# Performance work log

Hardware: AMD Instinct MI355X
Metric: run time of the kernel (lower is better)

The kernel has to match this reference:

```python
import jax, jax.numpy as jnp
import numpy as np

T, H, F, E, K = 1024, 2048, 1024, 8, 2  # tokens, hidden, intermediate, experts, top_k
RENORMALIZE = True


def setup_inputs() -> dict:
    key = jax.random.key(0)
    k1, k2, k3, k4, k5 = jax.random.split(key, 5)
    hidden_states = jax.random.normal(k1, (T, H), dtype=jnp.float32)
    router_logits = jax.random.normal(k2, (T, E), dtype=jnp.float32)
    w1 = jax.random.normal(k3, (E, H, F), dtype=jnp.float32) * 0.02  # gate proj
    w3 = jax.random.normal(k4, (E, H, F), dtype=jnp.float32) * 0.02  # up proj
    w2 = jax.random.normal(k5, (E, F, H), dtype=jnp.float32) * 0.02  # down proj
    return {"hidden_states": hidden_states, "router_logits": router_logits,
            "w1": w1, "w3": w3, "w2": w2}


def _moe_forward(x, router_logits, w1, w3, w2):
    # Top-K routing: softmax over all experts, select top-k, optional renormalize.
    probs = jax.nn.softmax(router_logits, axis=-1)            # [T, E]
    topk_vals, topk_ids = jax.lax.top_k(probs, K)             # [T, K]
    if RENORMALIZE:
        topk_vals = topk_vals / jnp.sum(topk_vals, axis=-1, keepdims=True)
    # Dense combine weights: zero for non-selected experts.   [T, E]
    tok_idx = jnp.arange(x.shape[0])[:, None]
    combine = jnp.zeros(probs.shape, dtype=x.dtype).at[tok_idx, topk_ids].set(topk_vals)
    # Expert SwiGLU FFN computed per expert over all tokens, masked-combined.
    g = jnp.einsum('th,ehf->etf', x, w1)                      # gate  [E, T, F]
    u = jnp.einsum('th,ehf->etf', x, w3)                      # up    [E, T, F]
    a = jax.nn.silu(g) * u                                    # silu activation
    y = jnp.einsum('etf,efh->eth', a, w2)                     # down  [E, T, H]
    out = jnp.einsum('eth,te->th', y, combine)                # weighted combine
    return out


def reference(hidden_states, router_logits, w1, w3, w2):
    return _moe_forward(hidden_states, router_logits, w1, w3, w2)
```

## Files before the change

### kernel.cpp

```cpp
#include <hip/hip_runtime.h>
#include <cstdint>
#include <cstddef>

#define T_TOK 1024
#define H_DIM 2048
#define F_DIM 1024
#define E_EXP 8
#define BM 64
#define BK 64
#define BN1 32
#define BN2 64
#define SP 70
#define MAX_TILES 40
#define ROWCAP 2560

#define I_NTILES 25
#define I_TILE_E 32
#define I_TILE_R0 80
#define I_ROWTOK 4224
#define I_ROWW   6784
#define B_XB     37888
#define B_AWS    (37888 + T_TOK*H_DIM*2)

typedef __bf16 bf16x8 __attribute__((ext_vector_type(8)));
typedef __bf16 bf16x4 __attribute__((ext_vector_type(4)));
typedef __bf16 bf16x2 __attribute__((ext_vector_type(2)));
typedef float  f32x4  __attribute__((ext_vector_type(4)));

#define MFMA(a,b,c) __builtin_amdgcn_mfma_f32_16x16x32_bf16(a,b,c,0,0,0)

__global__ __launch_bounds__(1024) void k_route(const float* __restrict__ logits,
                                                int* __restrict__ ws_i) {
  __shared__ int cnt[E_EXP], cur[E_EXP], offs_s[E_EXP];
  const int t = threadIdx.x;
  float* ws_f = (float*)ws_i;
  if (t < E_EXP) { cnt[t] = 0; cur[t] = 0; }
  __syncthreads();
  float l[E_EXP];
#pragma unroll
  for (int e = 0; e < E_EXP; ++e) l[e] = logits[t * E_EXP + e];
  int b0 = 0; float v0 = l[0];
#pragma unroll
  for (int e = 1; e < E_EXP; ++e) if (l[e] > v0) { v0 = l[e]; b0 = e; }
  int b1 = -1; float v1 = -3.4e38f;
#pragma unroll
  for (int e = 0; e < E_EXP; ++e) if (e != b0 && l[e] > v1) { v1 = l[e]; b1 = e; }
  float w0 = 1.f / (1.f + __expf(v1 - v0));
  float w1 = 1.f - w0;
  atomicAdd(&cnt[b0], 1);
  atomicAdd(&cnt[b1], 1);
  __syncthreads();
  if (t == 0) {
    int off = 0, nt = 0;
    for (int e = 0; e < E_EXP; ++e) {
      offs_s[e] = off;
      int ntile = (cnt[e] + BM - 1) / BM;
      for (int i = 0; i < ntile; ++i) {
        ws_i[I_TILE_E + nt] = e;
        ws_i[I_TILE_R0 + nt] = off + i * BM;
        ++nt;
      }
      off += ntile * BM;
    }
    ws_i[I_NTILES] = nt;
  }
  for (int i = t; i < ROWCAP; i += 1024) ws_i[I_ROWTOK + i] = -1;
  __syncthreads();
  {
    int p = atomicAdd(&cur[b0], 1);
    int s = offs_s[b0] + p;
    ws_i[I_ROWTOK + s] = t;
    ws_f[I_ROWW + s] = w0;
  }
  {
    int p = atomicAdd(&cur[b1], 1);
    int s = offs_s[b1] + p;
    ws_i[I_ROWTOK + s] = t;
    ws_f[I_ROWW + s] = w1;
  }
}

__global__ __launch_bounds__(256) void k_cvt(const float* __restrict__ x,
                                             __bf16* __restrict__ xb) {
  long i = (long)(blockIdx.x * 256 + threadIdx.x) * 8;
  float4 a = *(const float4*)(x + i);
  float4 b = *(const float4*)(x + i + 4);
  bf16x8 v;
  v[0] = (__bf16)a.x; v[1] = (__bf16)a.y; v[2] = (__bf16)a.z; v[3] = (__bf16)a.w;
  v[4] = (__bf16)b.x; v[5] = (__bf16)b.y; v[6] = (__bf16)b.z; v[7] = (__bf16)b.w;
  *(bf16x8*)(xb + i) = v;
}

__global__ __launch_bounds__(256) void k_gemm1(const __bf16* __restrict__ xb,
                                               const float* __restrict__ w1,
                                               const float* __restrict__ w3,
                                               const int* __restrict__ ws_i,
                                               __bf16* __restrict__ aws) {
  __shared__ __bf16 As[BM][SP];
  __shared__ __bf16 B1s[BN1][SP];
  __shared__ __bf16 B3s[BN1][SP];
  __shared__ int s_tok[BM];
  const int p = blockIdx.x;
  const int lg = (p & 7) * 160 + (p >> 3);
  const int tile = lg % MAX_TILES;
  const int n0 = (lg / MAX_TILES) * BN1;
  if (tile >= ws_i[I_NTILES]) return;
  const int e  = ws_i[I_TILE_E + tile];
  const int r0 = ws_i[I_TILE_R0 + tile];
  const int tid = threadIdx.x, lane = tid & 63, wid = tid >> 6;
  const int wm = wid;
  const int l15 = lane & 15, lk8 = (lane >> 4) << 3;
  const int ar = tid >> 3, ac = (tid & 7) * 8;
  const int nb = (tid & 7) * 4, kq = (tid >> 3) * 2;
  if (tid < BM) {
    int tk = ws_i[I_ROWTOK + r0 + tid];
    s_tok[tid] = tk < 0 ? 0 : tk;
  }
  __syncthreads();
  const int tok0 = s_tok[ar], tok1 = s_tok[ar + 32];
  const __bf16* xA0 = xb + (size_t)tok0 * H_DIM + ac;
  const __bf16* xA1 = xb + (size_t)tok1 * H_DIM + ac;
  const float* pB1 = w1 + (size_t)e * H_DIM * F_DIM + n0 + nb + (size_t)kq * F_DIM;
  const float* pB3 = w3 + (size_t)e * H_DIM * F_DIM + n0 + nb + (size_t)kq * F_DIM;

  bf16x8 rA0, rA1;
  f32x4 q1[2], q3[2];
  f32x4 accg[2] = {}; f32x4 accu[2] = {};

  auto LOADG = [&](int K0) {
    rA0 = *(const bf16x8*)(xA0 + K0);
    rA1 = *(const bf16x8*)(xA1 + K0);
#pragma unroll
    for (int j = 0; j < 2; ++j) {
      q1[j] = *(const f32x4*)(pB1 + (size_t)(K0 + j) * F_DIM);
      q3[j] = *(const f32x4*)(pB3 + (size_t)(K0 + j) * F_DIM);
    }
  };
  auto WRITEL = [&]() {
    *(bf16x8*)&As[ar][ac] = rA0;
    *(bf16x8*)&As[ar + 32][ac] = rA1;
#pragma unroll
    for (int u = 0; u < 4; ++u) {
      bf16x2 v1, v3;
      v1[0] = (__bf16)q1[0][u]; v1[1] = (__bf16)q1[1][u];
      v3[0] = (__bf16)q3[0][u]; v3[1] = (__bf16)q3[1][u];
      *(bf16x2*)&B1s[nb + u][kq] = v1;
      *(bf16x2*)&B3s[nb + u][kq] = v3;
    }
  };

  LOADG(0);
  for (int k0 = 0; k0 < H_DIM; k0 += BK) {
    if (k0) __syncthreads();
    WRITEL();
    if (k0 + BK < H_DIM) LOADG(k0 + BK);
    __syncthreads();
    __builtin_amdgcn_s_setprio(1);
#pragma unroll
    for (int kk = 0; kk < 2; ++kk) {
      const int kb = kk * 32 + lk8;
      bf16x8 a   = *(const bf16x8*)&As[wm * 16 + l15][kb];
      bf16x8 b10 = *(const bf16x8*)&B1s[l15][kb];
      bf16x8 b11 = *(const bf16x8*)&B1s[16 + l15][kb];
      bf16x8 b30 = *(const bf16x8*)&B3s[l15][kb];
      bf16x8 b31 = *(const bf16x8*)&B3s[16 + l15][kb];
      accg[0] = MFMA(a, b10, accg[0]);
      accg[1] = MFMA(a, b11, accg[1]);
      accu[0] = MFMA(a, b30, accu[0]);
      accu[1] = MFMA(a, b31, accu[1]);
    }
    __builtin_amdgcn_s_setprio(0);
  }
#pragma unroll
  for (int fn = 0; fn < 2; ++fn)
#pragma unroll
    for (int r = 0; r < 4; ++r) {
      float g = accg[fn][r], u = accu[fn][r];
      float a = g / (1.f + __expf(-g)) * u;
      int row = r0 + wm * 16 + ((lane >> 4) << 2) + r;
      int col = n0 + fn * 16 + l15;
      aws[(size_t)row * F_DIM + col] = (__bf16)a;
    }
}

__global__ __launch_bounds__(256) void k_gemm2(const __bf16* __restrict__ aws,
                                               const float* __restrict__ w2,
                                               const int* __restrict__ ws_i,
                                               float* __restrict__ out) {
  __shared__ __bf16 As[BM][SP];
  __shared__ __bf16 Bs[BN2][SP];
  __shared__ int s_tok[BM];
  __shared__ float s_w[BM];
  const int p = blockIdx.x;
  const int lg = (p & 7) * 160 + (p >> 3);
  const int tile = lg % MAX_TILES;
  const int h0 = (lg / MAX_TILES) * BN2;
  if (tile >= ws_i[I_NTILES]) return;
  const int e  = ws_i[I_TILE_E + tile];
  const int r0 = ws_i[I_TILE_R0 + tile];
  const int tid = threadIdx.x, lane = tid & 63, wid = tid >> 6;
  const int wm = wid >> 1, wn = wid & 1;
  const int l15 = lane & 15, lk8 = (lane >> 4) << 3;
  const int ar = tid >> 3, ac = (tid & 7) * 8;
  const int nb = (tid & 15) * 4, kq = (tid >> 4) * 4;
  const float* ws_f = (const float*)ws_i;
  if (tid < BM) {
    s_tok[tid] = ws_i[I_ROWTOK + r0 + tid];
    s_w[tid]   = ws_f[I_ROWW + r0 + tid];
  }
  __syncthreads();
  const __bf16* pA0 = aws + (size_t)(r0 + ar) * F_DIM + ac;
  const __bf16* pA1 = aws + (size_t)(r0 + ar + 32) * F_DIM + ac;
  const float* pB2 = w2 + (size_t)e * F_DIM * H_DIM + h0 + nb + (size_t)kq * H_DIM;

  bf16x8 rA0, rA1;
  f32x4 q2[4];
  auto LOADG = [&](int K0) {
    rA0 = *(const bf16x8*)(pA0 + K0);
    rA1 = *(const bf16x8*)(pA1 + K0);
#pragma unroll
    for (int j = 0; j < 4; ++j) q2[j] = *(const f32x4*)(pB2 + (size_t)(K0 + j) * H_DIM);
  };
  auto WRITEL = [&]() {
    *(bf16x8*)&As[ar][ac] = rA0;
    *(bf16x8*)&As[ar + 32][ac] = rA1;
#pragma unroll
    for (int u = 0; u < 4; ++u) {
      bf16x2 va, vb;
      va[0] = (__bf16)q2[0][u]; va[1] = (__bf16)q2[1][u];
      vb[0] = (__bf16)q2[2][u]; vb[1] = (__bf16)q2[3][u];
      *(bf16x2*)&Bs[nb + u][kq] = va;
      *(bf16x2*)&Bs[nb + u][kq + 2] = vb;
    }
  };

  f32x4 acc[2][2] = {};
  LOADG(0);
  for (int k0 = 0; k0 < F_DIM; k0 += BK) {
    if (k0) __syncthreads();
    WRITEL();
    if (k0 + BK < F_DIM) LOADG(k0 + BK);
    __syncthreads();
    __builtin_amdgcn_s_setprio(1);
#pragma unroll
    for (int kk = 0; kk < 2; ++kk) {
      const int kb = kk * 32 + lk8;
      bf16x8 a0 = *(const bf16x8*)&As[wm * 32 + l15][kb];
      bf16x8 a1 = *(const bf16x8*)&As[wm * 32 + 16 + l15][kb];
      bf16x8 b0 = *(const bf16x8*)&Bs[wn * 32 + l15][kb];
      bf16x8 b1 = *(const bf16x8*)&Bs[wn * 32 + 16 + l15][kb];
      acc[0][0] = MFMA(a0, b0, acc[0][0]);
      acc[0][1] = MFMA(a0, b1, acc[0][1]);
      acc[1][0] = MFMA(a1, b0, acc[1][0]);
      acc[1][1] = MFMA(a1, b1, acc[1][1]);
    }
    __builtin_amdgcn_s_setprio(0);
  }
#pragma unroll
  for (int fm = 0; fm < 2; ++fm)
#pragma unroll
    for (int fn = 0; fn < 2; ++fn)
#pragma unroll
      for (int r = 0; r < 4; ++r) {
        int lrow = wm * 32 + fm * 16 + ((lane >> 4) << 2) + r;
        int t = s_tok[lrow];
        if (t >= 0) {
          float v = acc[fm][fn][r] * s_w[lrow];
          atomicAdd(out + (size_t)t * H_DIM + h0 + wn * 32 + fn * 16 + l15, v);
        }
      }
}

extern "C" void kernel_launch(void* const* d_in, const int* in_sizes, int n_in,
                              void* d_out, int out_size, void* d_ws, size_t ws_size,
                              hipStream_t stream) {
  (void)in_sizes; (void)n_in; (void)out_size; (void)ws_size;
  const float* x      = (const float*)d_in[0];
  const float* logits = (const float*)d_in[1];
  const float* w1     = (const float*)d_in[2];
  const float* w3     = (const float*)d_in[3];
  const float* w2     = (const float*)d_in[4];
  float* out = (float*)d_out;
  int* ws_i = (int*)d_ws;
  __bf16* xb  = (__bf16*)((char*)d_ws + B_XB);
  __bf16* aws = (__bf16*)((char*)d_ws + B_AWS);

  hipMemsetAsync(d_out, 0, (size_t)T_TOK * H_DIM * sizeof(float), stream);
  k_route<<<1, 1024, 0, stream>>>(logits, ws_i);
  k_cvt<<<dim3(T_TOK * H_DIM / (256 * 8)), 256, 0, stream>>>(x, xb);
  k_gemm1<<<dim3(MAX_TILES * (F_DIM / BN1)), 256, 0, stream>>>(xb, w1, w3, ws_i, aws);
  k_gemm2<<<dim3(MAX_TILES * (H_DIM / BN2)), 256, 0, stream>>>(aws, w2, ws_i, out);
}
```

Measured before the change: 122.5 us.

## Pre-transpose gate/up weights to bf16 and use async LDS-loaded double-buffered GEMM1

Two new k_cvtT launches convert w1 and w3 from fp32 to bf16 and transpose them to [E,F,H] in workspace on every call. GEMM1 then stages the A and B tiles with global_load_lds straight into double-buffered, XOR-swizzled shared memory. Its output tile grows from 64x32 to 64x64, with a 2x2 warp layout and four MFMAs per operand pair. This removes the per-tile fp32 load, convert and LDS-store work and halves how often weight tiles are re-read. The cost is an extra full pass over both weight tensors every call: roughly 128 MB read and 64 MB written, plus more workspace.

```diff
diff --git a/kernel.cpp b/kernel.cpp
--- a/kernel.cpp
+++ b/kernel.cpp
@@ -8,7 +8,6 @@
 #define E_EXP 8
 #define BM 64
 #define BK 64
-#define BN1 32
 #define BN2 64
 #define SP 70
 #define MAX_TILES 40
@@ -20,14 +19,21 @@
 #define I_ROWTOK 4224
 #define I_ROWW   6784
 #define B_XB     37888
-#define B_AWS    (37888 + T_TOK*H_DIM*2)
+#define B_AWS    (B_XB + T_TOK*H_DIM*2)
+#define B_W1T    (B_AWS + ROWCAP*F_DIM*2)
+#define B_W3T    (B_W1T + E_EXP*F_DIM*H_DIM*2)
 
 typedef __bf16 bf16x8 __attribute__((ext_vector_type(8)));
-typedef __bf16 bf16x4 __attribute__((ext_vector_type(4)));
 typedef __bf16 bf16x2 __attribute__((ext_vector_type(2)));
 typedef float  f32x4  __attribute__((ext_vector_type(4)));
 
 #define MFMA(a,b,c) __builtin_amdgcn_mfma_f32_16x16x32_bf16(a,b,c,0,0,0)
+
+__device__ __forceinline__ void gload16(const void* g, void* l) {
+  __builtin_amdgcn_global_load_lds(
+      (const __attribute__((address_space(1))) void*)g,
+      (__attribute__((address_space(3))) void*)l, 16, 0, 0);
+}
 
 __global__ __launch_bounds__(1024) void k_route(const float* __restrict__ logits,
                                                 int* __restrict__ ws_i) {
@@ -91,96 +97,127 @@
   *(bf16x8*)(xb + i) = v;
 }
 
+__global__ __launch_bounds__(256) void k_cvtT(const float* __restrict__ src,
+                                              __bf16* __restrict__ dst,
+                                              int R, int C) {
+  __shared__ __bf16 tr[64][66];
+  const int e = blockIdx.z, r0 = blockIdx.x * 64, c0 = blockIdx.y * 64;
+  const float* s = src + ((size_t)e * R + r0) * C + c0;
+  __bf16* d = dst + ((size_t)e * C + c0) * R + r0;
+  const int t = threadIdx.x;
+  const int lr = t >> 4, lc = (t & 15) * 4;
+#pragma unroll
+  for (int i = 0; i < 4; ++i) {
+    int r = lr + i * 16;
+    float4 f = *(const float4*)(s + (size_t)r * C + lc);
+    tr[lc + 0][r] = (__bf16)f.x;
+    tr[lc + 1][r] = (__bf16)f.y;
+    tr[lc + 2][r] = (__bf16)f.z;
+    tr[lc + 3][r] = (__bf16)f.w;
+  }
+  __syncthreads();
+  const int oc = t >> 2, ok = (t & 3) * 16;
+  *(bf16x8*)(d + (size_t)oc * R + ok)     = *(const bf16x8*)&tr[oc][ok];
+  *(bf16x8*)(d + (size_t)oc * R + ok + 8) = *(const bf16x8*)&tr[oc][ok + 8];
+}
+
 __global__ __launch_bounds__(256) void k_gemm1(const __bf16* __restrict__ xb,
-                                               const float* __restrict__ w1,
-                                               const float* __restrict__ w3,
+                                               const __bf16* __restrict__ w1t,
+                                               const __bf16* __restrict__ w3t,
                                                const int* __restrict__ ws_i,
                                                __bf16* __restrict__ aws) {
-  __shared__ __bf16 As[BM][SP];
-  __shared__ __bf16 B1s[BN1][SP];
-  __shared__ __bf16 B3s[BN1][SP];
+  __shared__ __bf16 sm[2][3 * 4096];
   __shared__ int s_tok[BM];
   const int p = blockIdx.x;
-  const int lg = (p & 7) * 160 + (p >> 3);
+  const int lg = (p & 7) * 80 + (p >> 3);
   const int tile = lg % MAX_TILES;
-  const int n0 = (lg / MAX_TILES) * BN1;
+  const int n0 = (lg / MAX_TILES) * 64;
   if (tile >= ws_i[I_NTILES]) return;
   const int e  = ws_i[I_TILE_E + tile];
   const int r0 = ws_i[I_TILE_R0 + tile];
   const int tid = threadIdx.x, lane = tid & 63, wid = tid >> 6;
-  const int wm = wid;
-  const int l15 = lane & 15, lk8 = (lane >> 4) << 3;
-  const int ar = tid >> 3, ac = (tid & 7) * 8;
-  const int nb = (tid & 7) * 4, kq = (tid >> 3) * 2;
+  const int wm = wid >> 1, wn = wid & 1;
+  const int l15 = lane & 15, l4 = lane >> 4;
   if (tid < BM) {
     int tk = ws_i[I_ROWTOK + r0 + tid];
     s_tok[tid] = tk < 0 ? 0 : tk;
   }
   __syncthreads();
-  const int tok0 = s_tok[ar], tok1 = s_tok[ar + 32];
-  const __bf16* xA0 = xb + (size_t)tok0 * H_DIM + ac;
-  const __bf16* xA1 = xb + (size_t)tok1 * H_DIM + ac;
-  const float* pB1 = w1 + (size_t)e * H_DIM * F_DIM + n0 + nb + (size_t)kq * F_DIM;
-  const float* pB3 = w3 + (size_t)e * H_DIM * F_DIM + n0 + nb + (size_t)kq * F_DIM;
-
-  bf16x8 rA0, rA1;
-  f32x4 q1[2], q3[2];
-  f32x4 accg[2] = {}; f32x4 accu[2] = {};
-
-  auto LOADG = [&](int K0) {
-    rA0 = *(const bf16x8*)(xA0 + K0);
-    rA1 = *(const bf16x8*)(xA1 + K0);
-#pragma unroll
-    for (int j = 0; j < 2; ++j) {
-      q1[j] = *(const f32x4*)(pB1 + (size_t)(K0 + j) * F_DIM);
-      q3[j] = *(const f32x4*)(pB3 + (size_t)(K0 + j) * F_DIM);
-    }
+  const int rj0 = wid * 16 + (lane >> 3);
+  const int rj1 = rj0 + 8;
+  const int ks = ((lane & 7) ^ (lane >> 3)) * 8;
+  const __bf16* gA0 = xb + (size_t)s_tok[rj0] * H_DIM + ks;
+  const __bf16* gA1 = xb + (size_t)s_tok[rj1] * H_DIM + ks;
+  const __bf16* w1e = w1t + (size_t)e * F_DIM * H_DIM;
+  const __bf16* w3e = w3t + (size_t)e * F_DIM * H_DIM;
+  const __bf16* gB1_0 = w1e + (size_t)(n0 + rj0) * H_DIM + ks;
+  const __bf16* gB1_1 = w1e + (size_t)(n0 + rj1) * H_DIM + ks;
+  const __bf16* gB3_0 = w3e + (size_t)(n0 + rj0) * H_DIM + ks;
+  const __bf16* gB3_1 = w3e + (size_t)(n0 + rj1) * H_DIM + ks;
+  const int c0 = wid * 2 * 512, c1 = c0 + 512;
+
+  auto STAGE = [&](int b, int k0) {
+    __bf16* As = &sm[b][0];
+    __bf16* B1 = &sm[b][4096];
+    __bf16* B3 = &sm[b][8192];
+    gload16(gA0 + k0,   As + c0);
+    gload16(gA1 + k0,   As + c1);
+    gload16(gB1_0 + k0, B1 + c0);
+    gload16(gB1_1 + k0, B1 + c1);
+    gload16(gB3_0 + k0, B3 + c0);
+    gload16(gB3_1 + k0, B3 + c1);
   };
-  auto WRITEL = [&]() {
-    *(bf16x8*)&As[ar][ac] = rA0;
-    *(bf16x8*)&As[ar + 32][ac] = rA1;
-#pragma unroll
-    for (int u = 0; u < 4; ++u) {
-      bf16x2 v1, v3;
-      v1[0] = (__bf16)q1[0][u]; v1[1] = (__bf16)q1[1][u];
-      v3[0] = (__bf16)q3[0][u]; v3[1] = (__bf16)q3[1][u];
-      *(bf16x2*)&B1s[nb + u][kq] = v1;
-      *(bf16x2*)&B3s[nb + u][kq] = v3;
-    }
-  };
-
-  LOADG(0);
-  for (int k0 = 0; k0 < H_DIM; k0 += BK) {
-    if (k0) __syncthreads();
-    WRITEL();
-    if (k0 + BK < H_DIM) LOADG(k0 + BK);
-    __syncthreads();
+
+  f32x4 accg[2][2] = {}; f32x4 accu[2][2] = {};
+  auto COMPUTE = [&](int b) {
+    const __bf16* As = &sm[b][0];
+    const __bf16* B1 = &sm[b][4096];
+    const __bf16* B3 = &sm[b][8192];
     __builtin_amdgcn_s_setprio(1);
 #pragma unroll
     for (int kk = 0; kk < 2; ++kk) {
-      const int kb = kk * 32 + lk8;
-      bf16x8 a   = *(const bf16x8*)&As[wm * 16 + l15][kb];
-      bf16x8 b10 = *(const bf16x8*)&B1s[l15][kb];
-      bf16x8 b11 = *(const bf16x8*)&B1s[16 + l15][kb];
-      bf16x8 b30 = *(const bf16x8*)&B3s[l15][kb];
-      bf16x8 b31 = *(const bf16x8*)&B3s[16 + l15][kb];
-      accg[0] = MFMA(a, b10, accg[0]);
-      accg[1] = MFMA(a, b11, accg[1]);
-      accu[0] = MFMA(a, b30, accu[0]);
-      accu[1] = MFMA(a, b31, accu[1]);
+      const int sx = ((kk * 4 + l4) ^ (lane & 7)) << 3;
+      const int ra0 = wm * 32 + l15, ra1 = ra0 + 16;
+      const int rb0 = wn * 32 + l15, rb1 = rb0 + 16;
+      bf16x8 a0  = *(const bf16x8*)&As[ra0 * 64 + sx];
+      bf16x8 a1  = *(const bf16x8*)&As[ra1 * 64 + sx];
+      bf16x8 b10 = *(const bf16x8*)&B1[rb0 * 64 + sx];
+      bf16x8 b11 = *(const bf16x8*)&B1[rb1 * 64 + sx];
+      bf16x8 b30 = *(const bf16x8*)&B3[rb0 * 64 + sx];
+      bf16x8 b31 = *(const bf16x8*)&B3[rb1 * 64 + sx];
+      accg[0][0] = MFMA(a0, b10, accg[0][0]);
+      accg[0][1] = MFMA(a0, b11, accg[0][1]);
+      accg[1][0] = MFMA(a1, b10, accg[1][0]);
+      accg[1][1] = MFMA(a1, b11, accg[1][1]);
+      accu[0][0] = MFMA(a0, b30, accu[0][0]);
+      accu[0][1] = MFMA(a0, b31, accu[0][1]);
+      accu[1][0] = MFMA(a1, b30, accu[1][0]);
+      accu[1][1] = MFMA(a1, b31, accu[1][1]);
     }
     __builtin_amdgcn_s_setprio(0);
-  }
-#pragma unroll
-  for (int fn = 0; fn < 2; ++fn)
-#pragma unroll
-    for (int r = 0; r < 4; ++r) {
-      float g = accg[fn][r], u = accu[fn][r];
-      float a = g / (1.f + __expf(-g)) * u;
-      int row = r0 + wm * 16 + ((lane >> 4) << 2) + r;
-      int col = n0 + fn * 16 + l15;
-      aws[(size_t)row * F_DIM + col] = (__bf16)a;
-    }
+  };
+
+  STAGE(0, 0);
+  __syncthreads();
+  int curb = 0;
+  for (int t = 0; t < H_DIM / BK; ++t) {
+    if (t + 1 < H_DIM / BK) STAGE(curb ^ 1, (t + 1) * BK);
+    COMPUTE(curb);
+    __syncthreads();
+    curb ^= 1;
+  }
+#pragma unroll
+  for (int fm = 0; fm < 2; ++fm)
+#pragma unroll
+    for (int fn = 0; fn < 2; ++fn)
+#pragma unroll
+      for (int r = 0; r < 4; ++r) {
+        float g = accg[fm][fn][r], u = accu[fm][fn][r];
+        float a = g / (1.f + __expf(-g)) * u;
+        int row = r0 + wm * 32 + fm * 16 + l4 * 4 + r;
+        int col = n0 + wn * 32 + fn * 16 + l15;
+        aws[(size_t)row * F_DIM + col] = (__bf16)a;
+      }
 }
 
 __global__ __launch_bounds__(256) void k_gemm2(const __bf16* __restrict__ aws,
@@ -284,10 +321,14 @@
   int* ws_i = (int*)d_ws;
   __bf16* xb  = (__bf16*)((char*)d_ws + B_XB);
   __bf16* aws = (__bf16*)((char*)d_ws + B_AWS);
+  __bf16* w1t = (__bf16*)((char*)d_ws + B_W1T);
+  __bf16* w3t = (__bf16*)((char*)d_ws + B_W3T);
 
   hipMemsetAsync(d_out, 0, (size_t)T_TOK * H_DIM * sizeof(float), stream);
   k_route<<<1, 1024, 0, stream>>>(logits, ws_i);
   k_cvt<<<dim3(T_TOK * H_DIM / (256 * 8)), 256, 0, stream>>>(x, xb);
-  k_gemm1<<<dim3(MAX_TILES * (F_DIM / BN1)), 256, 0, stream>>>(xb, w1, w3, ws_i, aws);
+  k_cvtT<<<dim3(H_DIM / 64, F_DIM / 64, E_EXP), 256, 0, stream>>>(w1, w1t, H_DIM, F_DIM);
+  k_cvtT<<<dim3(H_DIM / 64, F_DIM / 64, E_EXP), 256, 0, stream>>>(w3, w3t, H_DIM, F_DIM);
+  k_gemm1<<<dim3(MAX_TILES * (F_DIM / 64)), 256, 0, stream>>>(xb, w1t, w3t, ws_i, aws);
   k_gemm2<<<dim3(MAX_TILES * (H_DIM / BN2)), 256, 0, stream>>>(aws, w2, ws_i, out);
 }
```

Result: slower. 126.7 us (+3.4%).
